# Performance work log

Hardware: AMD Instinct MI355X
Metric: run time of the kernel (lower is better)

The kernel has to match this reference:

```python
import jax, jax.numpy as jnp
import numpy as np

B, C, H, W = 4, 256, 64, 64
GROUPS = 32
EPS = 1e-5


def setup_inputs() -> dict:
    key = jax.random.key(0)
    ks = jax.random.split(key, 8)
    s = 1.0 / np.sqrt(C)
    return {
        "Hand": jax.random.normal(ks[0], (B, C, H, W), jnp.float32),
        "U": jax.random.normal(ks[1], (B, C, H, W), jnp.float32),
        "WH_w": jax.random.normal(ks[2], (C, C), jnp.float32) * s,
        "WH_b": jax.random.normal(ks[3], (C,), jnp.float32) * 0.01,
        "WU_w": jax.random.normal(ks[4], (C, C), jnp.float32) * s,
        "WU_b": jax.random.normal(ks[5], (C,), jnp.float32) * 0.01,
        "gn_w": jax.random.normal(ks[6], (C,), jnp.float32) * 0.1,
        "gn_b": jax.random.normal(ks[7], (C,), jnp.float32) * 0.1,
    }


def _group_norm(x, w, b):
    # x: [B, C, H, W], normalize within each of GROUPS channel groups over (C//G, H, W)
    b_, c_, h_, w_ = x.shape
    xg = x.reshape(b_, GROUPS, c_ // GROUPS, h_, w_)
    mean = jnp.mean(xg, axis=(2, 3, 4), keepdims=True)
    var = jnp.var(xg, axis=(2, 3, 4), keepdims=True)
    xn = ((xg - mean) * jax.lax.rsqrt(var + EPS)).reshape(b_, c_, h_, w_)
    return xn * w[None, :, None, None] + b[None, :, None, None]


def reference(Hand, U, WH_w, WH_b, WU_w, WU_b, gn_w, gn_b):
    b_, c_, h_, w_ = Hand.shape
    n = h_ * w_
    Hf = Hand.reshape(b_, c_, n)  # [B, C, N]
    Uf = U.reshape(b_, c_, n)     # [B, C, N]
    # 1x1 convs == per-pixel linear on channels
    q = jnp.einsum('oc,bcn->bon', WH_w, Hf) + WH_b[None, :, None]  # [B, C, N]
    k = jnp.einsum('oc,bcn->bon', WU_w, Uf) + WU_b[None, :, None]  # [B, C, N]
    # affinity: A[b, n, m] = sum_c q[b,c,n] * k[b,c,m]  (unscaled)
    A = jnp.einsum('bcn,bcm->bnm', q, k)  # [B, N, N]
    A = jax.nn.softmax(A, axis=-1)
    out = jnp.einsum('bnm,bcm->bcn', A, Uf).reshape(b_, c_, h_, w_)
    return _group_norm(out, gn_w, gn_b) + Hand
```

## Files before the change

kernel.cpp:

```cpp
#include <hip/hip_runtime.h>
#include <hip/hip_fp16.h>
#include <math.h>


typedef _Float16 v8h __attribute__((ext_vector_type(8)));
typedef float    v4f __attribute__((ext_vector_type(4)));

#define NB 4
#define NC 256
#define NS 4096
#define NG 32
#define GEPS 1e-5f
#define NSPLIT 3
#define KSTRIDE 272
#define KTILE   8704
#define PSTRIDE 40

#define ASYNC_BARRIER() asm volatile("s_waitcnt lgkmcnt(0)\n\ts_barrier" ::: "memory")

template <int CTRL>
__device__ __forceinline__ float dpp_rot(float x) {
    int r = __builtin_amdgcn_update_dpp(__float_as_int(x), __float_as_int(x),
                                        CTRL, 0xF, 0xF, false);
    return __int_as_float(r);
}
__device__ __forceinline__ float row_max16(float x) {
    x = fmaxf(x, dpp_rot<0x128>(x));
    x = fmaxf(x, dpp_rot<0x124>(x));
    x = fmaxf(x, dpp_rot<0x122>(x));
    x = fmaxf(x, dpp_rot<0x121>(x));
    return x;
}
__device__ __forceinline__ float row_sum16(float x) {
    x = x + dpp_rot<0x128>(x);
    x = x + dpp_rot<0x124>(x);
    x = x + dpp_rot<0x122>(x);
    x = x + dpp_rot<0x121>(x);
    return x;
}

__global__ __launch_bounds__(256) void k_convert(const float* __restrict__ Wh,
    const float* __restrict__ Wu, _Float16* __restrict__ Wh16, _Float16* __restrict__ Wu16)
{
    const int i = blockIdx.x * 256 + threadIdx.x;
    const int o = i >> 8, c = i & 255;
    const int idx = ((((o >> 4) * 8 + (c >> 5)) * 4 + ((c >> 3) & 3)) * 16
                     + (o & 15)) * 8 + (c & 7);
    Wh16[idx] = (_Float16)Wh[i];
    Wu16[idx] = (_Float16)Wu[i];
}

__global__ __launch_bounds__(256) void k_qkgemm(const float* __restrict__ Hand,
    const float* __restrict__ U, const _Float16* __restrict__ Wh16,
    const _Float16* __restrict__ Wu16, const float* __restrict__ WHb,
    const float* __restrict__ WUb, _Float16* __restrict__ qT,
    _Float16* __restrict__ kTsw, _Float16* __restrict__ Uh)
{
    const int nt = blockIdx.x, b = blockIdx.y, z = blockIdx.z;
    const float*    X    = z ? U    : Hand;
    const _Float16* W    = z ? Wu16 : Wh16;
    const float*    bias = z ? WUb  : WHb;

    const int tid = threadIdx.x, w = tid >> 6, lane = tid & 63;
    const int q4 = lane >> 4, l15 = lane & 15;
    const int n = nt * 64 + w * 16 + l15;

    const float* Xcol = X + (size_t)b * NC * NS + n;
    v8h A[8];
#pragma unroll
    for (int kc = 0; kc < 8; ++kc) {
        const int c0 = kc * 32 + q4 * 8;
        v8h a;
#pragma unroll
        for (int j = 0; j < 8; ++j) a[j] = (_Float16)Xcol[(size_t)(c0 + j) * NS];
        A[kc] = a;
    }

    if (z == 1) {
        _Float16* ub = Uh + (size_t)b * NC * NS + n;
#pragma unroll
        for (int kc = 0; kc < 8; ++kc) {
            const int c0 = kc * 32 + q4 * 8;
#pragma unroll
            for (int j = 0; j < 8; ++j) ub[(size_t)(c0 + j) * NS] = A[kc][j];
        }
    }

#pragma unroll 4
    for (int osub = 0; osub < 16; ++osub) {
        const int o = osub * 16 + l15;
        v4f acc = {0.f, 0.f, 0.f, 0.f};
#pragma unroll
        for (int kc = 0; kc < 8; ++kc) {
            const v8h bf = *(const v8h*)(W + ((size_t)(osub * 8 + kc) * 64 + lane) * 8);
            acc = __builtin_amdgcn_mfma_f32_16x16x32_f16(A[kc], bf, acc, 0, 0, 0);
        }
        const float bv = bias[o];
        if (z == 0) {
            _Float16* orow = qT + ((size_t)b * NS + nt * 64 + w * 16 + q4 * 4) * NC + o;
#pragma unroll
            for (int r = 0; r < 4; ++r) orow[(size_t)r * NC] = (_Float16)(acc[r] + bv);
        } else {
            _Float16* kb = kTsw + (size_t)b * 128 * KTILE;
#pragma unroll
            for (int r = 0; r < 4; ++r) {
                const int m = nt * 64 + w * 16 + q4 * 4 + r;
                kb[(size_t)(m >> 5) * KTILE + (m & 31) * KSTRIDE + o] = (_Float16)(acc[r] + bv);
            }
        }
    }
}

__global__ __launch_bounds__(256, 3) void k_attn(const _Float16* __restrict__ qT,
    const _Float16* __restrict__ kTsw, const _Float16* __restrict__ Uh,
    _Float16* __restrict__ Ppart, float* __restrict__ mstat, float* __restrict__ lstat)
{
    const int b  = blockIdx.x;
    const int nt = blockIdx.y;
    const int s  = blockIdx.z;
    const int t0 = (s == 0) ? 0 : (s == 1 ? 43 : 86);
    const int t1 = (s == 2) ? 128 : t0 + 43;

    __shared__ __align__(16) _Float16 Klds[2][KTILE];
    __shared__ __align__(16) _Float16 Plds[64 * PSTRIDE];
    __shared__ __align__(16) float alphaS[64];

    const int tid = threadIdx.x, w = tid >> 6, lane = tid & 63;
    const int q4 = lane >> 4, l15 = lane & 15;

    const _Float16* kTb = kTsw + (size_t)b * 128 * KTILE;
    const _Float16* Uhb = Uh + (size_t)b * NC * NS;

    {
        const _Float16* src = kTb + (size_t)t0 * KTILE;
#pragma unroll
        for (int j = 0; j < 5; ++j) {
            const int ch = (w * 5 + j) % 17;
            __builtin_amdgcn_global_load_lds(
                (const __attribute__((address_space(1))) void*)(src + ch * 512 + lane * 8),
                (__attribute__((address_space(3))) void*)(&Klds[t0 & 1][ch * 512]), 16, 0, 0);
        }
    }

    v8h Q[8];
    {
        const _Float16* qrow = qT + ((size_t)b * NS + nt * 64 + w * 16 + l15) * NC;
#pragma unroll
        for (int kc = 0; kc < 8; ++kc) Q[kc] = *(const v8h*)(qrow + kc * 32 + q4 * 8);
    }

    v4f O[4][4];
#pragma unroll
    for (int i = 0; i < 4; ++i)
#pragma unroll
        for (int j = 0; j < 4; ++j) O[i][j] = (v4f){0.f, 0.f, 0.f, 0.f};
    float mi[4] = {-INFINITY, -INFINITY, -INFINITY, -INFINITY};
    float li[4] = {0.f, 0.f, 0.f, 0.f};

    for (int t = t0; t < t1; ++t) {
        const int p = t & 1;
        const int m0 = t * 32;

        v8h Ur[4];
#pragma unroll
        for (int js = 0; js < 4; ++js)
            Ur[js] = *(const v8h*)(Uhb + (size_t)(w * 64 + js * 16 + l15) * NS + m0 + q4 * 8);
        asm volatile("" ::: "memory");

        {
            const int tn = (t + 1 < t1) ? t + 1 : t0;
            const _Float16* src = kTb + (size_t)tn * KTILE;
#pragma unroll
            for (int j = 0; j < 5; ++j) {
                const int ch = (w * 5 + j) % 17;
                __builtin_amdgcn_global_load_lds(
                    (const __attribute__((address_space(1))) void*)(src + ch * 512 + lane * 8),
                    (__attribute__((address_space(3))) void*)(&Klds[p ^ 1][ch * 512]), 16, 0, 0);
            }
        }

        asm volatile("s_waitcnt vmcnt(9)" ::: "memory");
        ASYNC_BARRIER();

        v4f sv[2];
        sv[0] = (v4f){0.f, 0.f, 0.f, 0.f};
        sv[1] = (v4f){0.f, 0.f, 0.f, 0.f};
#pragma unroll
        for (int kc = 0; kc < 8; ++kc) {
#pragma unroll
            for (int ms = 0; ms < 2; ++ms) {
                const v8h kf = *(const v8h*)(&Klds[p][(ms * 16 + l15) * KSTRIDE
                                             + (kc * 4 + q4) * 8]);
                sv[ms] = __builtin_amdgcn_mfma_f32_16x16x32_f16(Q[kc], kf, sv[ms], 0, 0, 0);
            }
        }

        float al[4];
#pragma unroll
        for (int r = 0; r < 4; ++r) {
            const float tm = row_max16(fmaxf(sv[0][r], sv[1][r]));
            const float mn = fmaxf(mi[r], tm);
            al[r] = __expf(mi[r] - mn);
            mi[r] = mn;
            const float p0 = __expf(sv[0][r] - mn);
            const float p1 = __expf(sv[1][r] - mn);
            sv[0][r] = p0; sv[1][r] = p1;
            li[r] = li[r] * al[r] + p0 + p1;
        }
        if (l15 == 0) {
#pragma unroll
            for (int r = 0; r < 4; ++r) alphaS[w * 16 + q4 * 4 + r] = al[r];
        }
#pragma unroll
        for (int ms = 0; ms < 2; ++ms)
#pragma unroll
            for (int r = 0; r < 4; ++r) {
                const int row = w * 16 + q4 * 4 + r;
                Plds[row * PSTRIDE + ms * 16 + l15] = (_Float16)sv[ms][r];
            }
        ASYNC_BARRIER();

#pragma unroll
        for (int is = 0; is < 4; ++is) {
            const float4 av = *(const float4*)&alphaS[is * 16 + q4 * 4];
            const v4f aa = {av.x, av.y, av.z, av.w};
#pragma unroll
            for (int js = 0; js < 4; ++js) O[is][js] *= aa;
        }
#pragma unroll
        for (int is = 0; is < 4; ++is) {
            const v8h Pf = *(const v8h*)(&Plds[(is * 16 + l15) * PSTRIDE + q4 * 8]);
#pragma unroll
            for (int js = 0; js < 4; ++js)
                O[is][js] = __builtin_amdgcn_mfma_f32_16x16x32_f16(Pf, Ur[js], O[is][js], 0, 0, 0);
        }
    }

    asm volatile("s_waitcnt vmcnt(0)" ::: "memory");

#pragma unroll
    for (int r = 0; r < 4; ++r) li[r] = row_sum16(li[r]);
    if (l15 == 0) {
#pragma unroll
        for (int r = 0; r < 4; ++r) {
            const int n = nt * 64 + w * 16 + q4 * 4 + r;
            mstat[(size_t)(s * NB + b) * NS + n] = mi[r];
            lstat[(size_t)(s * NB + b) * NS + n] = li[r];
        }
    }
#pragma unroll
    for (int is = 0; is < 4; ++is)
#pragma unroll
        for (int js = 0; js < 4; ++js)
#pragma unroll
            for (int r = 0; r < 4; ++r) {
                _Float16* dst = Ppart + ((size_t)(s * NB + b) * NS + nt * 64 + is * 16
                                         + q4 * 4 + r) * NC + w * 64 + js * 16 + l15;
                __builtin_nontemporal_store((_Float16)O[is][js][r], dst);
            }
}

__global__ __launch_bounds__(256) void k_merge(const _Float16* __restrict__ Pp,
    const float* __restrict__ mstat, const float* __restrict__ lstat,
    float* __restrict__ Opre, float* __restrict__ statacc)
{
    const int b = blockIdx.y, tid = threadIdx.x;
    const int n = blockIdx.x * 8 + (tid >> 5);
    const int c0 = (tid & 31) * 8;
    const size_t nb = (size_t)b * NS + n;
    const size_t SP = (size_t)NB * NS;
    const float m0 = mstat[nb], m1 = mstat[SP + nb], m2 = mstat[2 * SP + nb];
    const float l0 = lstat[nb], l1 = lstat[SP + nb], l2 = lstat[2 * SP + nb];
    const float M  = fmaxf(m0, fmaxf(m1, m2));
    const float e0 = __expf(m0 - M), e1 = __expf(m1 - M), e2 = __expf(m2 - M);
    const float inv = 1.f / (e0 * l0 + e1 * l1 + e2 * l2);
    const float w0 = e0 * inv, w1 = e1 * inv, w2 = e2 * inv;
    const size_t base = nb * NC + c0;
    const v8h p0 = *(const v8h*)(Pp + base);
    const v8h p1 = *(const v8h*)(Pp + SP * NC + base);
    const v8h p2 = *(const v8h*)(Pp + 2 * SP * NC + base);
    float v[8];
    float s1 = 0.f, s2 = 0.f;
#pragma unroll
    for (int j = 0; j < 8; ++j) {
        v[j] = w0 * (float)p0[j] + w1 * (float)p1[j] + w2 * (float)p2[j];
        s1 += v[j]; s2 += v[j] * v[j];
    }
    *(float4*)(Opre + base)     = make_float4(v[0], v[1], v[2], v[3]);
    *(float4*)(Opre + base + 4) = make_float4(v[4], v[5], v[6], v[7]);

    __shared__ float r1[256], r2[256];
    r1[tid] = s1; r2[tid] = s2;
    __syncthreads();
    if (tid < 32) {
        float a = 0.f, q = 0.f;
#pragma unroll
        for (int k = 0; k < 8; ++k) { a += r1[tid + 32 * k]; q += r2[tid + 32 * k]; }
        atomicAdd(&statacc[(b * NG + tid) * 2 + 0], a);
        atomicAdd(&statacc[(b * NG + tid) * 2 + 1], q);
    }
}

__global__ __launch_bounds__(256) void k_gnapply(const float* __restrict__ Opre,
    const float* __restrict__ Hand, const float* __restrict__ gnw,
    const float* __restrict__ gnb, const float* __restrict__ statacc,
    float* __restrict__ out)
{
    const int nt = blockIdx.x, ct = blockIdx.y, b = blockIdx.z;
    __shared__ float buf[64 * 65];
    const int tid = threadIdx.x;
    {
        const int nr = tid >> 4, c4 = (tid & 15) * 4;
#pragma unroll
        for (int k = 0; k < 4; ++k) {
            const int n = nr + 16 * k;
            const float4 v = *(const float4*)(Opre + ((size_t)b * NS + nt * 64 + n) * NC
                                              + ct * 64 + c4);
            buf[n * 65 + c4 + 0] = v.x; buf[n * 65 + c4 + 1] = v.y;
            buf[n * 65 + c4 + 2] = v.z; buf[n * 65 + c4 + 3] = v.w;
        }
    }
    __syncthreads();
    const int nw = tid & 63, c0 = tid >> 6;
#pragma unroll
    for (int k = 0; k < 16; ++k) {
        const int cl = c0 + 4 * k;
        const int c  = ct * 64 + cl;
        const int g  = c >> 3;
        const float s1   = statacc[(b * NG + g) * 2 + 0];
        const float s2   = statacc[(b * NG + g) * 2 + 1];
        const float mean = s1 * (1.f / 32768.f);
        const float var  = s2 * (1.f / 32768.f) - mean * mean;
        const float rstd = rsqrtf(var + GEPS);
        const size_t oidx = ((size_t)b * NC + c) * NS + nt * 64 + nw;
        out[oidx] = (buf[nw * 65 + cl] - mean) * rstd * gnw[c] + gnb[c] + Hand[oidx];
    }
}

extern "C" void kernel_launch(void* const* d_in, const int* in_sizes, int n_in,
                              void* d_out, int out_size, void* d_ws, size_t ws_size,
                              hipStream_t stream)
{
    const float* Hand = (const float*)d_in[0];
    const float* U    = (const float*)d_in[1];
    const float* WHw  = (const float*)d_in[2];
    const float* WHb  = (const float*)d_in[3];
    const float* WUw  = (const float*)d_in[4];
    const float* WUb  = (const float*)d_in[5];
    const float* gnw  = (const float*)d_in[6];
    const float* gnb  = (const float*)d_in[7];
    float* out = (float*)d_out;

    char* ws = (char*)d_ws;
    _Float16* qT     = (_Float16*)(ws);
    _Float16* kTsw   = (_Float16*)(ws + 8388608);
    _Float16* Uh     = (_Float16*)(ws + 17301504);
    _Float16* Wh16   = (_Float16*)(ws + 25690112);
    _Float16* Wu16   = (_Float16*)(ws + 25821184);
    float*    mstat  = (float*)(ws + 25952256);
    float*    lstat  = (float*)(ws + 26148864);
    float*    statacc= (float*)(ws + 26345472);
    _Float16* Ppart  = (_Float16*)(ws + 26347520);
    float*    Opre   = (float*)(ws);

    hipMemsetAsync(statacc, 0, NB * NG * 2 * sizeof(float), stream);
    k_convert<<<dim3((NC * NC) / 256), 256, 0, stream>>>(WHw, WUw, Wh16, Wu16);
    k_qkgemm <<<dim3(64, NB, 2), 256, 0, stream>>>(Hand, U, Wh16, Wu16, WHb, WUb, qT, kTsw, Uh);
    k_attn   <<<dim3(NB, 64, NSPLIT), 256, 0, stream>>>(qT, kTsw, Uh, Ppart, mstat, lstat);
    k_merge  <<<dim3(NS / 8, NB), 256, 0, stream>>>(Ppart, mstat, lstat, Opre, statacc);
    k_gnapply<<<dim3(64, 4, NB), 256, 0, stream>>>(Opre, Hand, gnw, gnb, statacc, out);
}
```

Measured before the change: 276.1 us.

## Split attention into four equal KV chunks and store merged output in fp16

The attention kernel's key split goes from three uneven chunks (43/43/42 tiles) to four equal 32-tile chunks, with launch bounds raised to four blocks per CU. This gives more blocks and balances the work across them. The merge kernel now combines four partials and writes the merged result as fp16 in place over the first partial buffer, instead of a separate fp32 buffer. This halves the traffic between merge and group-norm apply, at the cost of an extra partial to write and read, fp16 rounding before normalization, and a higher register-pressure limit in k_attn.

Result: slower. 388.7 us (+40.8%).

```diff
diff --git a/kernel.cpp b/kernel.cpp
--- a/kernel.cpp
+++ b/kernel.cpp
@@ -4,6 +4,7 @@
 
 
 typedef _Float16 v8h __attribute__((ext_vector_type(8)));
+typedef _Float16 v4h __attribute__((ext_vector_type(4)));
 typedef float    v4f __attribute__((ext_vector_type(4)));
 
 #define NB 4
@@ -11,7 +12,7 @@
 #define NS 4096
 #define NG 32
 #define GEPS 1e-5f
-#define NSPLIT 3
+#define NSPLIT 4
 #define KSTRIDE 272
 #define KTILE   8704
 #define PSTRIDE 40
@@ -111,15 +112,15 @@
     }
 }
 
-__global__ __launch_bounds__(256, 3) void k_attn(const _Float16* __restrict__ qT,
+__global__ __launch_bounds__(256, 4) void k_attn(const _Float16* __restrict__ qT,
     const _Float16* __restrict__ kTsw, const _Float16* __restrict__ Uh,
     _Float16* __restrict__ Ppart, float* __restrict__ mstat, float* __restrict__ lstat)
 {
     const int b  = blockIdx.x;
     const int nt = blockIdx.y;
     const int s  = blockIdx.z;
-    const int t0 = (s == 0) ? 0 : (s == 1 ? 43 : 86);
-    const int t1 = (s == 2) ? 128 : t0 + 43;
+    const int t0 = s * 32;
+    const int t1 = t0 + 32;
 
     __shared__ __align__(16) _Float16 Klds[2][KTILE];
     __shared__ __align__(16) _Float16 Plds[64 * PSTRIDE];
@@ -260,34 +261,39 @@
             }
 }
 
-__global__ __launch_bounds__(256) void k_merge(const _Float16* __restrict__ Pp,
+__global__ __launch_bounds__(256) void k_merge(_Float16* __restrict__ Pp,
     const float* __restrict__ mstat, const float* __restrict__ lstat,
-    float* __restrict__ Opre, float* __restrict__ statacc)
+    float* __restrict__ statacc)
 {
     const int b = blockIdx.y, tid = threadIdx.x;
     const int n = blockIdx.x * 8 + (tid >> 5);
     const int c0 = (tid & 31) * 8;
     const size_t nb = (size_t)b * NS + n;
     const size_t SP = (size_t)NB * NS;
-    const float m0 = mstat[nb], m1 = mstat[SP + nb], m2 = mstat[2 * SP + nb];
-    const float l0 = lstat[nb], l1 = lstat[SP + nb], l2 = lstat[2 * SP + nb];
-    const float M  = fmaxf(m0, fmaxf(m1, m2));
-    const float e0 = __expf(m0 - M), e1 = __expf(m1 - M), e2 = __expf(m2 - M);
-    const float inv = 1.f / (e0 * l0 + e1 * l1 + e2 * l2);
-    const float w0 = e0 * inv, w1 = e1 * inv, w2 = e2 * inv;
+    const float m0 = mstat[nb],          m1 = mstat[SP + nb];
+    const float m2 = mstat[2 * SP + nb], m3 = mstat[3 * SP + nb];
+    const float l0 = lstat[nb],          l1 = lstat[SP + nb];
+    const float l2 = lstat[2 * SP + nb], l3 = lstat[3 * SP + nb];
+    const float M  = fmaxf(fmaxf(m0, m1), fmaxf(m2, m3));
+    const float e0 = __expf(m0 - M), e1 = __expf(m1 - M);
+    const float e2 = __expf(m2 - M), e3 = __expf(m3 - M);
+    const float inv = 1.f / (e0 * l0 + e1 * l1 + e2 * l2 + e3 * l3);
+    const float w0 = e0 * inv, w1 = e1 * inv, w2 = e2 * inv, w3 = e3 * inv;
     const size_t base = nb * NC + c0;
     const v8h p0 = *(const v8h*)(Pp + base);
     const v8h p1 = *(const v8h*)(Pp + SP * NC + base);
     const v8h p2 = *(const v8h*)(Pp + 2 * SP * NC + base);
-    float v[8];
+    const v8h p3 = *(const v8h*)(Pp + 3 * SP * NC + base);
     float s1 = 0.f, s2 = 0.f;
+    v8h hm;
 #pragma unroll
     for (int j = 0; j < 8; ++j) {
-        v[j] = w0 * (float)p0[j] + w1 * (float)p1[j] + w2 * (float)p2[j];
-        s1 += v[j]; s2 += v[j] * v[j];
-    }
-    *(float4*)(Opre + base)     = make_float4(v[0], v[1], v[2], v[3]);
-    *(float4*)(Opre + base + 4) = make_float4(v[4], v[5], v[6], v[7]);
+        const float v = w0 * (float)p0[j] + w1 * (float)p1[j]
+                      + w2 * (float)p2[j] + w3 * (float)p3[j];
+        s1 += v; s2 += v * v;
+        hm[j] = (_Float16)v;
+    }
+    *(v8h*)(Pp + base) = hm;
 
     __shared__ float r1[256], r2[256];
     r1[tid] = s1; r2[tid] = s2;
@@ -301,7 +307,7 @@
     }
 }
 
-__global__ __launch_bounds__(256) void k_gnapply(const float* __restrict__ Opre,
+__global__ __launch_bounds__(256) void k_gnapply(const _Float16* __restrict__ Om,
     const float* __restrict__ Hand, const float* __restrict__ gnw,
     const float* __restrict__ gnb, const float* __restrict__ statacc,
     float* __restrict__ out)
@@ -314,10 +320,10 @@
 #pragma unroll
         for (int k = 0; k < 4; ++k) {
             const int n = nr + 16 * k;
-            const float4 v = *(const float4*)(Opre + ((size_t)b * NS + nt * 64 + n) * NC
-                                              + ct * 64 + c4);
-            buf[n * 65 + c4 + 0] = v.x; buf[n * 65 + c4 + 1] = v.y;
-            buf[n * 65 + c4 + 2] = v.z; buf[n * 65 + c4 + 3] = v.w;
+            const v4h v = *(const v4h*)(Om + ((size_t)b * NS + nt * 64 + n) * NC
+                                        + ct * 64 + c4);
+            buf[n * 65 + c4 + 0] = (float)v[0]; buf[n * 65 + c4 + 1] = (float)v[1];
+            buf[n * 65 + c4 + 2] = (float)v[2]; buf[n * 65 + c4 + 3] = (float)v[3];
         }
     }
     __syncthreads();
@@ -358,15 +364,14 @@
     _Float16* Wh16   = (_Float16*)(ws + 25690112);
     _Float16* Wu16   = (_Float16*)(ws + 25821184);
     float*    mstat  = (float*)(ws + 25952256);
-    float*    lstat  = (float*)(ws + 26148864);
-    float*    statacc= (float*)(ws + 26345472);
-    _Float16* Ppart  = (_Float16*)(ws + 26347520);
-    float*    Opre   = (float*)(ws);
+    float*    lstat  = (float*)(ws + 26214400);
+    float*    statacc= (float*)(ws + 26476544);
+    _Float16* Ppart  = (_Float16*)(ws + 26478592);
 
     hipMemsetAsync(statacc, 0, NB * NG * 2 * sizeof(float), stream);
     k_convert<<<dim3((NC * NC) / 256), 256, 0, stream>>>(WHw, WUw, Wh16, Wu16);
     k_qkgemm <<<dim3(64, NB, 2), 256, 0, stream>>>(Hand, U, Wh16, Wu16, WHb, WUb, qT, kTsw, Uh);
     k_attn   <<<dim3(NB, 64, NSPLIT), 256, 0, stream>>>(qT, kTsw, Uh, Ppart, mstat, lstat);
-    k_merge  <<<dim3(NS / 8, NB), 256, 0, stream>>>(Ppart, mstat, lstat, Opre, statacc);
-    k_gnapply<<<dim3(64, 4, NB), 256, 0, stream>>>(Opre, Hand, gnw, gnb, statacc, out);
-}
+    k_merge  <<<dim3(NS / 8, NB), 256, 0, stream>>>(Ppart, mstat, lstat, statacc);
+    k_gnapply<<<dim3(64, 4, NB), 256, 0, stream>>>(Ppart, Hand, gnw, gnb, statacc, out);
+}
```
